# Performance work log

Measured on AMD Instinct MI355X. Metric: run time of the kernel, lower is better.

The kernel has to match this reference:

```python
import jax, jax.numpy as jnp
import numpy as np

B = 1024
FEAT_C = [64, 64, 128, 256, 512]    # channel dim of each intermediate feature map
SPATIAL = [1024, 1024, 256, 64, 16]  # flattened HxW of each map (32x32 input)
STRIDES = [1, 1, 2, 4, 8]
NUM_CLASS = 10


def _conv(x, w, b, s):
    y = jax.lax.conv_general_dilated(x, w, (s, s), 'SAME',
                                     dimension_numbers=('NCHW', 'OIHW', 'NCHW'))
    return y + b[None, :, None, None]


def setup_inputs() -> dict:
    key = jax.random.key(0)
    ks = iter(jax.random.split(key, 64))
    nrm = lambda shape, scale=1.0: jax.random.normal(next(ks), shape, jnp.float32) * scale
    inp = {'x': nrm((B, 3, 32, 32))}
    inp['noise_w'] = nrm((15, 3, 3, 3), 0.1)
    inp['noise_b'] = nrm((15,), 0.01)
    for i, (c, s) in enumerate(zip(FEAT_C, SPATIAL)):
        inp[f'feat_w{i}'] = nrm((c, 3, 3, 3), 0.2)
        inp[f'feat_b{i}'] = nrm((c,), 0.01)
        inp[f'mu_w{i}'] = nrm((NUM_CLASS, s), 1.0 / np.sqrt(s))
        inp[f'mu_b{i}'] = nrm((NUM_CLASS,), 0.01)
        inp[f'std_w{i}'] = nrm((NUM_CLASS, s), 1.0 / np.sqrt(s))
        inp[f'std_b{i}'] = nrm((NUM_CLASS,), 0.01)
    inp['clf_w'] = nrm((1, 5), 0.5)
    inp['clf_b'] = nrm((1,), 0.01)
    return inp


def _forward(x, noise_w, noise_b, feat_ws, feat_bs, mu_ws, mu_bs, std_ws, std_bs, clf_w, clf_b):
    Bsz = x.shape[0]
    # noised_img = x.repeat([1,5,1,1]) + noise_layer(x)   -> [B,15,32,32]
    noised = jnp.tile(x, (1, 5, 1, 1)) + _conv(x, noise_w, noise_b, 1)
    ekey = jax.random.key(42)
    scores, means, stds = [], [], []
    for i in range(5):
        xi = noised[:, 3 * i:3 * (i + 1)]
        # stand-in for pretrained_model.intermediate_forward -> [B, C_i, S_i]
        f = _conv(xi, feat_ws[i], feat_bs[i], STRIDES[i]).reshape(Bsz, FEAT_C[i], -1)
        # Linear over flattened-spatial dim then transpose(1,2): [B, 10, C_i]
        x_mean = jnp.einsum('bcs,ks->bkc', f, mu_ws[i]) + mu_bs[i][None, :, None]
        x_std = jnp.einsum('bcs,ks->bkc', f, std_ws[i]) + std_bs[i][None, :, None]
        # original builds dense diag(std)^2 [B,10,C,C]; diagonal exploited analytically
        var = x_std * x_std                       # diag entries of x_variance (== scale_tril)
        eps = jax.random.normal(jax.random.fold_in(ekey, i), x_mean.shape, x_mean.dtype)
        d = var * eps                             # sample - mean = scale_tril @ eps (diagonal)
        # -0.5 * d^T inv(diag(var)) d, inverse done analytically instead of torch.inverse
        mahal = -0.5 * jnp.sum(d * d / var, axis=-1)   # [B, 10]
        idx = jnp.argmax(mahal, axis=1)
        scores.append(jnp.max(mahal, axis=1))
        means.append(jnp.take_along_axis(x_mean, idx[:, None, None], axis=1)[:, 0, :])
        stds.append(jnp.take_along_axis(x_std, idx[:, None, None], axis=1)[:, 0, :])
    score_stack = jnp.stack(scores, axis=1)       # [B, 5]
    out = (score_stack @ clf_w.T + clf_b)[:, 0]   # classifier Linear(5,1), squeeze(-1)
    return out, means, stds


def reference(x, noise_w, noise_b,
              feat_w0, feat_b0, mu_w0, mu_b0, std_w0, std_b0,
              feat_w1, feat_b1, mu_w1, mu_b1, std_w1, std_b1,
              feat_w2, feat_b2, mu_w2, mu_b2, std_w2, std_b2,
              feat_w3, feat_b3, mu_w3, mu_b3, std_w3, std_b3,
              feat_w4, feat_b4, mu_w4, mu_b4, std_w4, std_b4,
              clf_w, clf_b):
    feat_ws = [feat_w0, feat_w1, feat_w2, feat_w3, feat_w4]
    feat_bs = [feat_b0, feat_b1, feat_b2, feat_b3, feat_b4]
    mu_ws = [mu_w0, mu_w1, mu_w2, mu_w3, mu_w4]
    mu_bs = [mu_b0, mu_b1, mu_b2, mu_b3, mu_b4]
    std_ws = [std_w0, std_w1, std_w2, std_w3, std_w4]
    std_bs = [std_b0, std_b1, std_b2, std_b3, std_b4]
    out, means, stds = _forward(x, noise_w, noise_b, feat_ws, feat_bs,
                                mu_ws, mu_bs, std_ws, std_bs, clf_w, clf_b)
    return (out, *means, *stds)
```

## Files before the change

kernel.cpp:

```cpp
#include <hip/hip_runtime.h>
#include <cstdint>

#define B_SZ 1024

__host__ __device__ inline void tf2x32(uint32_t k0, uint32_t k1,
                                       uint32_t x0, uint32_t x1,
                                       uint32_t& o0, uint32_t& o1) {
  uint32_t ks2 = 0x1BD11BDAu ^ k0 ^ k1;
#define TF_RND(r) { x0 += x1; x1 = (x1 << (r)) | (x1 >> (32 - (r))); x1 ^= x0; }
  x0 += k0; x1 += k1;
  TF_RND(13) TF_RND(15) TF_RND(26) TF_RND(6)
  x0 += k1; x1 += ks2 + 1u;
  TF_RND(17) TF_RND(29) TF_RND(16) TF_RND(24)
  x0 += ks2; x1 += k0 + 2u;
  TF_RND(13) TF_RND(15) TF_RND(26) TF_RND(6)
  x0 += k0; x1 += k1 + 3u;
  TF_RND(17) TF_RND(29) TF_RND(16) TF_RND(24)
  x0 += k1; x1 += ks2 + 4u;
  TF_RND(13) TF_RND(15) TF_RND(26) TF_RND(6)
  x0 += ks2; x1 += k0 + 5u;
#undef TF_RND
  o0 = x0; o1 = x1;
}

__device__ inline float erfinv_f32(float x) {
  float w = -log1pf(-x * x);
  float p;
  if (w < 5.0f) {
    w -= 2.5f;
    p = 2.81022636e-08f;
    p = fmaf(p, w, 3.43273939e-07f);
    p = fmaf(p, w, -3.5233877e-06f);
    p = fmaf(p, w, -4.39150654e-06f);
    p = fmaf(p, w, 0.00021858087f);
    p = fmaf(p, w, -0.00125372503f);
    p = fmaf(p, w, -0.00417768164f);
    p = fmaf(p, w, 0.246640727f);
    p = fmaf(p, w, 1.50140941f);
  } else {
    w = sqrtf(w) - 3.0f;
    p = -0.000200214257f;
    p = fmaf(p, w, 0.000100950558f);
    p = fmaf(p, w, 0.00134934322f);
    p = fmaf(p, w, -0.00367342844f);
    p = fmaf(p, w, 0.00573950773f);
    p = fmaf(p, w, -0.0076224613f);
    p = fmaf(p, w, 0.00943887047f);
    p = fmaf(p, w, 1.00167406f);
    p = fmaf(p, w, 2.83297682f);
  }
  return p * x;
}

__device__ inline float jax_normal_pt(uint32_t k0, uint32_t k1, uint32_t e) {
  uint32_t o0, o1;
  tf2x32(k0, k1, 0u, e, o0, o1);
  uint32_t bits = o0 ^ o1;
  float f = __uint_as_float((bits >> 9) | 0x3f800000u) - 1.0f;
  const float LO = -0.99999994f;
  float u = fmaxf(LO, fmaf(f, 2.0f, LO));
  return 1.41421356f * erfinv_f32(u);
}

struct OodArgs {
  const float* x;
  const float* noise_w;
  const float* noise_b;
  const float* feat_w[5];
  const float* feat_b[5];
  const float* mu_w[5];
  const float* mu_b[5];
  const float* std_w[5];
  const float* std_b[5];
  float* mean_out[5];
  float* std_out[5];
  float* scores;
  float* gws;
  uint32_t fk0[5], fk1[5];
};

#define PITCH 35
#define CHSZ  (34 * PITCH)
#define XSZ   (3 * CHSZ)

#define A_XP   0
#define A_XI   3570
#define A_NW   7140
#define A_NB   7221
#define A_SMEM 7224

template<int S, int STRIDE>
__device__ __forceinline__ void stageA(const OodArgs& A_, float* smem, int i) {
  constexpr int Wd = 32 / STRIDE;

  const int b = blockIdx.x;
  const int t = threadIdx.x;

  float* s_xp = smem + A_XP;
  float* s_xi = smem + A_XI;
  float* s_nw = smem + A_NW;
  float* s_nb = smem + A_NB;

  for (int p = t; p < 2 * XSZ; p += 320) smem[p] = 0.0f;
  if (t < 81) s_nw[t] = A_.noise_w[81 * i + t];
  if (t < 3)  s_nb[t] = A_.noise_b[3 * i + t];
  __syncthreads();
  const float* xb = A_.x + (size_t)b * 3072;
  for (int p = t; p < 3072; p += 320) {
    int ci = p >> 10; int rr = p & 1023; int yy = rr >> 5; int xx = rr & 31;
    s_xp[ci * CHSZ + (yy + 1) * PITCH + (xx + 1)] = xb[p];
  }
  __syncthreads();

  #pragma unroll
  for (int co = 0; co < 3; ++co) {
    float nwr[27];
    #pragma unroll
    for (int j = 0; j < 27; ++j) nwr[j] = s_nw[co * 27 + j];
    const float nb = s_nb[co];
    for (int p = t; p < 1024; p += 320) {
      const int base = (p >> 5) * PITCH + (p & 31);
      float a = nb;
      #pragma unroll
      for (int c2 = 0; c2 < 3; ++c2) {
        #pragma unroll
        for (int q = 0; q < 9; ++q)
          a = fmaf(s_xp[c2 * CHSZ + base + (q / 3) * PITCH + (q % 3)],
                   nwr[c2 * 9 + q], a);
      }
      s_xi[co * CHSZ + base + PITCH + 1] = a + s_xp[co * CHSZ + base + PITCH + 1];
    }
  }
  __syncthreads();

  const int G  = t >> 4;
  const int ss = t & 15;
  const int wh = G & 1;
  const int kk = G >> 1;
  const float* wsrc = (wh ? A_.std_w[i] : A_.mu_w[i]) + kk * S;
  float* gdst = A_.gws + (size_t)(b * 5 + i) * 560;

  if constexpr (STRIDE == 1) {
    const float* wr = wsrc + (2 * ss) * 32;
    const int rbase0 = (2 * ss) * PITCH;
    #pragma unroll
    for (int ci = 0; ci < 3; ++ci) {
      const int rb = ci * CHSZ + rbase0;
      float acc[10];
      #pragma unroll
      for (int j = 0; j < 10; ++j) acc[j] = 0.0f;
      float Av[4], Bv[4], Cv[4];
      #pragma unroll
      for (int u = 0; u < 4; ++u) {
        Av[u] = s_xi[rb + u * PITCH + 0];
        Bv[u] = s_xi[rb + u * PITCH + 1];
      }

#define WCOMP(V, L) ((L) == 0 ? (V).x : (L) == 1 ? (V).y : (L) == 2 ? (V).z : (V).w)
#define STEP(X, P, Q, R, W0, W1) { \
    _Pragma("unroll") \
    for (int u = 0; u < 4; ++u) R[u] = s_xi[rb + u * PITCH + (X) + 2]; \
    const float w0c = WCOMP(W0, (X) & 3); \
    const float w1c = WCOMP(W1, (X) & 3); \
    _Pragma("unroll") \
    for (int dy = 0; dy < 3; ++dy) { \
      acc[dy*3+0] = fmaf(w0c, P[dy], fmaf(w1c, P[dy+1], acc[dy*3+0])); \
      acc[dy*3+1] = fmaf(w0c, Q[dy], fmaf(w1c, Q[dy+1], acc[dy*3+1])); \
      acc[dy*3+2] = fmaf(w0c, R[dy], fmaf(w1c, R[dy+1], acc[dy*3+2])); \
    } \
    if (ci == 0) acc[9] += w0c + w1c; \
  }
#define G4_0(c) { const float4 w0 = *(const float4*)(wr + (c)); \
                  const float4 w1 = *(const float4*)(wr + 32 + (c)); \
    STEP((c)+0, Av, Bv, Cv, w0, w1) STEP((c)+1, Bv, Cv, Av, w0, w1) \
    STEP((c)+2, Cv, Av, Bv, w0, w1) STEP((c)+3, Av, Bv, Cv, w0, w1) }
#define G4_1(c) { const float4 w0 = *(const float4*)(wr + (c)); \
                  const float4 w1 = *(const float4*)(wr + 32 + (c)); \
    STEP((c)+0, Bv, Cv, Av, w0, w1) STEP((c)+1, Cv, Av, Bv, w0, w1) \
    STEP((c)+2, Av, Bv, Cv, w0, w1) STEP((c)+3, Bv, Cv, Av, w0, w1) }
#define G4_2(c) { const float4 w0 = *(const float4*)(wr + (c)); \
                  const float4 w1 = *(const float4*)(wr + 32 + (c)); \
    STEP((c)+0, Cv, Av, Bv, w0, w1) STEP((c)+1, Av, Bv, Cv, w0, w1) \
    STEP((c)+2, Bv, Cv, Av, w0, w1) STEP((c)+3, Cv, Av, Bv, w0, w1) }

      G4_0(0) G4_1(4) G4_2(8) G4_0(12) G4_1(16) G4_2(20) G4_0(24) G4_1(28)

#undef G4_0
#undef G4_1
#undef G4_2
#undef STEP
#undef WCOMP
      #pragma unroll
      for (int j = 0; j < 10; ++j) {
        float v = acc[j];
        v += __shfl_xor(v, 1, 64);
        v += __shfl_xor(v, 2, 64);
        v += __shfl_xor(v, 4, 64);
        v += __shfl_xor(v, 8, 64);
        acc[j] = v;
      }
      if (ss == 0) {
        #pragma unroll
        for (int j = 0; j < 9; ++j)
          gdst[(wh * 10 + kk) * 27 + ci * 9 + j] = acc[j];
        if (ci == 0) gdst[540 + wh * 10 + kk] = acc[9];
      }
    }
  } else {
    constexpr int PER = S / 16;
    #pragma unroll
    for (int ci = 0; ci < 3; ++ci) {
      float acc[10];
      #pragma unroll
      for (int j = 0; j < 10; ++j) acc[j] = 0.0f;
      #pragma unroll
      for (int u = 0; u < PER; ++u) {
        const int s  = ss * PER + u;
        const int yo = s / Wd, xo = s % Wd;
        const float wx = wsrc[s];
        #pragma unroll
        for (int dy = 0; dy < 3; ++dy) {
          const int base = ci * CHSZ + (yo * STRIDE + dy + 1) * PITCH + (xo * STRIDE + 1);
          #pragma unroll
          for (int dx = 0; dx < 3; ++dx)
            acc[dy * 3 + dx] = fmaf(wx, s_xi[base + dx], acc[dy * 3 + dx]);
        }
        if (ci == 0) acc[9] += wx;
      }
      #pragma unroll
      for (int j = 0; j < 10; ++j) {
        float v = acc[j];
        v += __shfl_xor(v, 1, 64);
        v += __shfl_xor(v, 2, 64);
        v += __shfl_xor(v, 4, 64);
        v += __shfl_xor(v, 8, 64);
        acc[j] = v;
      }
      if (ss == 0) {
        #pragma unroll
        for (int j = 0; j < 9; ++j)
          gdst[(wh * 10 + kk) * 27 + ci * 9 + j] = acc[j];
        if (ci == 0) gdst[540 + wh * 10 + kk] = acc[9];
      }
    }
  }
}

__global__ __launch_bounds__(320, 8)
void ood_a(OodArgs A_) {
  __shared__ float smem[A_SMEM];
  const int y = blockIdx.y;
  switch (y) {
    case 0:
    case 1: stageA<1024, 1>(A_, smem, y); break;
    case 2: stageA< 256, 2>(A_, smem, 2); break;
    case 3: stageA<  64, 4>(A_, smem, 3); break;
    default: stageA< 16, 8>(A_, smem, 4); break;
  }
}

template<int I, int C>
__device__ __forceinline__ void stageB(const OodArgs& A_, float* smem) {
  const int b = blockIdx.x;
  const int t = threadIdx.x;

  float* s_g   = smem;
  float* s_rs  = smem + 540;
  float* s_std = smem + 560;
  float* s_pt  = smem + 560 + 10 * C;
  int*   s_idx = (int*)(smem + 570 + 10 * C);

  const float* feat_w = A_.feat_w[I];
  const float* feat_b = A_.feat_b[I];
  const uint32_t fk0 = A_.fk0[I], fk1 = A_.fk1[I];

  const float* gsrc = A_.gws + (size_t)(b * 5 + I) * 560;
  for (int p = t; p < 560; p += 320) smem[p] = gsrc[p];
  __syncthreads();

  for (int v = t; v < 10 * C; v += 320) {
    const int k2 = v / C; const int c = v - k2 * C;
    const float* fw = feat_w + c * 27;
    float a2 = 0.0f;
    #pragma unroll
    for (int j = 0; j < 27; ++j) a2 = fmaf(s_g[(10 + k2) * 27 + j], fw[j], a2);
    a2 = fmaf(feat_b[c], s_rs[10 + k2], a2) + A_.std_b[I][k2];
    s_std[v] = a2;
  }
  __syncthreads();

  {
    const int g  = t >> 6;
    const int ln = t & 63;
    float m0 = 0.0f, m1 = 0.0f;
    for (int c = ln; c < C; c += 64) {
      {
        const float sd  = s_std[g * C + c];
        const float eps = jax_normal_pt(fk0, fk1, (uint32_t)((b * 10 + g) * C + c));
        m0 = fmaf(sd * sd, eps * eps, m0);
      }
      {
        const float sd  = s_std[(g + 5) * C + c];
        const float eps = jax_normal_pt(fk0, fk1, (uint32_t)((b * 10 + g + 5) * C + c));
        m1 = fmaf(sd * sd, eps * eps, m1);
      }
    }
    #pragma unroll
    for (int off = 32; off > 0; off >>= 1) {
      m0 += __shfl_down(m0, off, 64);
      m1 += __shfl_down(m1, off, 64);
    }
    if (ln == 0) { s_pt[g] = m0; s_pt[g + 5] = m1; }
  }
  __syncthreads();
  if (t == 0) {
    float best = -INFINITY; int bi = 0;
    #pragma unroll
    for (int k2 = 0; k2 < 10; ++k2) {
      float m = -0.5f * s_pt[k2];
      if (m > best) { best = m; bi = k2; }
    }
    A_.scores[b * 5 + I] = best;
    *s_idx = bi;
  }
  __syncthreads();

  const int idx = *s_idx;
  for (int c = t; c < C; c += 320) {
    const float* fw = feat_w + c * 27;
    float a1 = 0.0f;
    #pragma unroll
    for (int j = 0; j < 27; ++j) a1 = fmaf(s_g[idx * 27 + j], fw[j], a1);
    a1 = fmaf(feat_b[c], s_rs[idx], a1) + A_.mu_b[I][idx];
    A_.mean_out[I][(size_t)b * C + c] = a1;
    A_.std_out[I][(size_t)b * C + c]  = s_std[idx * C + c];
  }
}

__global__ __launch_bounds__(320)
void ood_b(OodArgs A_) {
  __shared__ float smem[571 + 5120];
  switch (blockIdx.y) {
    case 0: stageB<0,  64>(A_, smem); break;
    case 1: stageB<1,  64>(A_, smem); break;
    case 2: stageB<2, 128>(A_, smem); break;
    case 3: stageB<3, 256>(A_, smem); break;
    default: stageB<4, 512>(A_, smem); break;
  }
}

__global__ void ood_clf(const float* __restrict__ scores,
                        const float* __restrict__ clf_w,
                        const float* __restrict__ clf_b,
                        float* __restrict__ out) {
  int b = blockIdx.x * blockDim.x + threadIdx.x;
  if (b < B_SZ) {
    float acc = clf_b[0];
    #pragma unroll
    for (int i = 0; i < 5; ++i) acc = fmaf(scores[b * 5 + i], clf_w[i], acc);
    out[b] = acc;
  }
}

extern "C" void kernel_launch(void* const* d_in, const int* in_sizes, int n_in,
                              void* d_out, int out_size, void* d_ws, size_t ws_size,
                              hipStream_t stream) {
  (void)in_sizes; (void)n_in; (void)out_size; (void)ws_size;
  const float* clf_w = (const float*)d_in[33];
  const float* clf_b = (const float*)d_in[34];
  float* out = (float*)d_out;
  float* ws  = (float*)d_ws;

  OodArgs A_;
  A_.x       = (const float*)d_in[0];
  A_.noise_w = (const float*)d_in[1];
  A_.noise_b = (const float*)d_in[2];
  const size_t NMEAN = 1048576;
  const size_t moff[5] = {1024, 66560, 132096, 263168, 525312};
  for (int i = 0; i < 5; ++i) {
    A_.feat_w[i]   = (const float*)d_in[3 + 6 * i];
    A_.feat_b[i]   = (const float*)d_in[4 + 6 * i];
    A_.mu_w[i]     = (const float*)d_in[5 + 6 * i];
    A_.mu_b[i]     = (const float*)d_in[6 + 6 * i];
    A_.std_w[i]    = (const float*)d_in[7 + 6 * i];
    A_.std_b[i]    = (const float*)d_in[8 + 6 * i];
    A_.mean_out[i] = out + moff[i];
    A_.std_out[i]  = out + moff[i] + NMEAN;
    tf2x32(0u, 42u, 0u, (uint32_t)i, A_.fk0[i], A_.fk1[i]);
  }
  A_.scores = ws;
  A_.gws    = ws + 5120;

  ood_a<<<dim3(B_SZ, 5), 320, 0, stream>>>(A_);
  ood_b<<<dim3(B_SZ, 5), 320, 0, stream>>>(A_);
  ood_clf<<<(B_SZ + 255) / 256, 256, 0, stream>>>(A_.scores, clf_w, clf_b, out);
}
```

Measured before the change: 322.4 us.

## Restructure noise conv, halve stage-A smem, fuse classifier into per-batch stage B

Stage A now does the noise conv in place in one image buffer, with 192 threads each computing 16 outputs in a register-rotating sliding window. The weighted-sum phase is remapped so each 32-lane group handles two classes at once and reuses the loaded pixels. Launch bounds drop from 8 to 5 blocks. Stage B becomes one block per batch element that loops over the five feature maps and computes the final classifier inline, removing the separate classifier kernel and the score buffer round-trip. This trades per-map parallelism in stage B (5x fewer blocks) for fewer launches and less shared memory in stage A.

```diff
diff --git a/kernel.cpp b/kernel.cpp
--- a/kernel.cpp
+++ b/kernel.cpp
@@ -72,9 +72,11 @@
   const float* mu_b[5];
   const float* std_w[5];
   const float* std_b[5];
+  const float* clf_w;
+  const float* clf_b;
   float* mean_out[5];
   float* std_out[5];
-  float* scores;
+  float* out;
   float* gws;
   uint32_t fk0[5], fk1[5];
 };
@@ -82,104 +84,155 @@
 #define PITCH 35
 #define CHSZ  (34 * PITCH)
 #define XSZ   (3 * CHSZ)
-
-#define A_XP   0
-#define A_XI   3570
-#define A_NW   7140
-#define A_NB   7221
-#define A_SMEM 7224
+#define A_NW   XSZ
+#define A_NB   (XSZ + 81)
+#define A_SMEM (XSZ + 84)
 
 template<int S, int STRIDE>
 __device__ __forceinline__ void stageA(const OodArgs& A_, float* smem, int i) {
   constexpr int Wd = 32 / STRIDE;
-
   const int b = blockIdx.x;
   const int t = threadIdx.x;
-
-  float* s_xp = smem + A_XP;
-  float* s_xi = smem + A_XI;
-  float* s_nw = smem + A_NW;
-  float* s_nb = smem + A_NB;
-
-  for (int p = t; p < 2 * XSZ; p += 320) smem[p] = 0.0f;
+  float* s_img = smem;
+  float* s_nw  = smem + A_NW;
+  float* s_nb  = smem + A_NB;
+
+  for (int p = t; p < XSZ; p += 320) s_img[p] = 0.0f;
   if (t < 81) s_nw[t] = A_.noise_w[81 * i + t];
   if (t < 3)  s_nb[t] = A_.noise_b[3 * i + t];
   __syncthreads();
   const float* xb = A_.x + (size_t)b * 3072;
   for (int p = t; p < 3072; p += 320) {
-    int ci = p >> 10; int rr = p & 1023; int yy = rr >> 5; int xx = rr & 31;
-    s_xp[ci * CHSZ + (yy + 1) * PITCH + (xx + 1)] = xb[p];
+    int ci = p >> 10, rr = p & 1023, yy = rr >> 5, xx = rr & 31;
+    s_img[ci * CHSZ + (yy + 1) * PITCH + (xx + 1)] = xb[p];
   }
   __syncthreads();
 
-  #pragma unroll
-  for (int co = 0; co < 3; ++co) {
-    float nwr[27];
-    #pragma unroll
-    for (int j = 0; j < 27; ++j) nwr[j] = s_nw[co * 27 + j];
+  float acc2[16];
+  int ob = 0;
+  const bool act = (t < 192);
+  if (act) {
+    const int co = t / 64, r = t % 64, y = r >> 1, xs = (r & 1) * 16;
+    ob = co * CHSZ + (y + 1) * PITCH + (xs + 1);
     const float nb = s_nb[co];
-    for (int p = t; p < 1024; p += 320) {
-      const int base = (p >> 5) * PITCH + (p & 31);
-      float a = nb;
-      #pragma unroll
-      for (int c2 = 0; c2 < 3; ++c2) {
-        #pragma unroll
-        for (int q = 0; q < 9; ++q)
-          a = fmaf(s_xp[c2 * CHSZ + base + (q / 3) * PITCH + (q % 3)],
-                   nwr[c2 * 9 + q], a);
-      }
-      s_xi[co * CHSZ + base + PITCH + 1] = a + s_xp[co * CHSZ + base + PITCH + 1];
+    #pragma unroll
+    for (int j = 0; j < 16; ++j) acc2[j] = nb;
+    #pragma unroll
+    for (int c2 = 0; c2 < 3; ++c2) {
+      float nwr[9];
+      #pragma unroll
+      for (int q = 0; q < 9; ++q) nwr[q] = s_nw[co * 27 + c2 * 9 + q];
+      const int wb = c2 * CHSZ + y * PITCH + xs;
+      float P[3], Q[3], R[3];
+      #pragma unroll
+      for (int d = 0; d < 3; ++d) {
+        P[d] = s_img[wb + d * PITCH];
+        Q[d] = s_img[wb + d * PITCH + 1];
+      }
+#define CSTEP(J, P_, Q_, R_) { \
+      _Pragma("unroll") \
+      for (int d = 0; d < 3; ++d) R_[d] = s_img[wb + d * PITCH + (J) + 2]; \
+      _Pragma("unroll") \
+      for (int d = 0; d < 3; ++d) { \
+        acc2[J] = fmaf(nwr[d*3+0], P_[d], acc2[J]); \
+        acc2[J] = fmaf(nwr[d*3+1], Q_[d], acc2[J]); \
+        acc2[J] = fmaf(nwr[d*3+2], R_[d], acc2[J]); \
+      } }
+      CSTEP(0,P,Q,R)  CSTEP(1,Q,R,P)  CSTEP(2,R,P,Q)
+      CSTEP(3,P,Q,R)  CSTEP(4,Q,R,P)  CSTEP(5,R,P,Q)
+      CSTEP(6,P,Q,R)  CSTEP(7,Q,R,P)  CSTEP(8,R,P,Q)
+      CSTEP(9,P,Q,R)  CSTEP(10,Q,R,P) CSTEP(11,R,P,Q)
+      CSTEP(12,P,Q,R) CSTEP(13,Q,R,P) CSTEP(14,R,P,Q)
+      CSTEP(15,P,Q,R)
+#undef CSTEP
     }
   }
   __syncthreads();
-
-  const int G  = t >> 4;
-  const int ss = t & 15;
-  const int wh = G & 1;
-  const int kk = G >> 1;
-  const float* wsrc = (wh ? A_.std_w[i] : A_.mu_w[i]) + kk * S;
+  if (act) {
+    #pragma unroll
+    for (int j = 0; j < 16; ++j) {
+      const float v = acc2[j] + s_img[ob + j];
+      s_img[ob + j] = v;
+    }
+  }
+  __syncthreads();
+
+  const int g  = t >> 5;
+  const int ss = t & 31;
+  const int wh = g & 1;
+  const int k0 = (g >> 1) * 2;
+  const float* wbase = (wh ? A_.std_w[i] : A_.mu_w[i]) + k0 * S;
   float* gdst = A_.gws + (size_t)(b * 5 + i) * 560;
 
+#define REDUCE_WRITE(ci_) { \
+    _Pragma("unroll") \
+    for (int j = 0; j < 9; ++j) { \
+      float v0 = a0[j], v1 = a1[j]; \
+      v0 += __shfl_xor(v0, 1, 64);  v1 += __shfl_xor(v1, 1, 64); \
+      v0 += __shfl_xor(v0, 2, 64);  v1 += __shfl_xor(v1, 2, 64); \
+      v0 += __shfl_xor(v0, 4, 64);  v1 += __shfl_xor(v1, 4, 64); \
+      v0 += __shfl_xor(v0, 8, 64);  v1 += __shfl_xor(v1, 8, 64); \
+      v0 += __shfl_xor(v0, 16, 64); v1 += __shfl_xor(v1, 16, 64); \
+      a0[j] = v0; a1[j] = v1; \
+    } \
+    if ((ci_) == 0) { \
+      rs0 += __shfl_xor(rs0, 1, 64); rs0 += __shfl_xor(rs0, 2, 64); \
+      rs0 += __shfl_xor(rs0, 4, 64); rs0 += __shfl_xor(rs0, 8, 64); \
+      rs0 += __shfl_xor(rs0, 16, 64); \
+      rs1 += __shfl_xor(rs1, 1, 64); rs1 += __shfl_xor(rs1, 2, 64); \
+      rs1 += __shfl_xor(rs1, 4, 64); rs1 += __shfl_xor(rs1, 8, 64); \
+      rs1 += __shfl_xor(rs1, 16, 64); \
+    } \
+    if (ss == 0) { \
+      _Pragma("unroll") \
+      for (int j = 0; j < 9; ++j) { \
+        gdst[(wh * 10 + k0) * 27 + (ci_) * 9 + j]     = a0[j]; \
+        gdst[(wh * 10 + k0 + 1) * 27 + (ci_) * 9 + j] = a1[j]; \
+      } \
+      if ((ci_) == 0) { \
+        gdst[540 + wh * 10 + k0]     = rs0; \
+        gdst[540 + wh * 10 + k0 + 1] = rs1; \
+      } \
+    } }
+
   if constexpr (STRIDE == 1) {
-    const float* wr = wsrc + (2 * ss) * 32;
-    const int rbase0 = (2 * ss) * PITCH;
+    const float* wr = wbase + ss * 32;
     #pragma unroll
     for (int ci = 0; ci < 3; ++ci) {
-      const int rb = ci * CHSZ + rbase0;
-      float acc[10];
-      #pragma unroll
-      for (int j = 0; j < 10; ++j) acc[j] = 0.0f;
-      float Av[4], Bv[4], Cv[4];
-      #pragma unroll
-      for (int u = 0; u < 4; ++u) {
-        Av[u] = s_xi[rb + u * PITCH + 0];
-        Bv[u] = s_xi[rb + u * PITCH + 1];
-      }
-
+      const int rb = ci * CHSZ + ss * PITCH;
+      float a0[9], a1[9];
+      #pragma unroll
+      for (int j = 0; j < 9; ++j) { a0[j] = 0.0f; a1[j] = 0.0f; }
+      float rs0 = 0.0f, rs1 = 0.0f;
+      float Av[3], Bv[3], Cv[3];
+      #pragma unroll
+      for (int u = 0; u < 3; ++u) {
+        Av[u] = s_img[rb + u * PITCH];
+        Bv[u] = s_img[rb + u * PITCH + 1];
+      }
 #define WCOMP(V, L) ((L) == 0 ? (V).x : (L) == 1 ? (V).y : (L) == 2 ? (V).z : (V).w)
-#define STEP(X, P, Q, R, W0, W1) { \
+#define STEP(X, P_, Q_, R_, W0, W1) { \
     _Pragma("unroll") \
-    for (int u = 0; u < 4; ++u) R[u] = s_xi[rb + u * PITCH + (X) + 2]; \
+    for (int u = 0; u < 3; ++u) R_[u] = s_img[rb + u * PITCH + (X) + 2]; \
     const float w0c = WCOMP(W0, (X) & 3); \
     const float w1c = WCOMP(W1, (X) & 3); \
     _Pragma("unroll") \
     for (int dy = 0; dy < 3; ++dy) { \
-      acc[dy*3+0] = fmaf(w0c, P[dy], fmaf(w1c, P[dy+1], acc[dy*3+0])); \
-      acc[dy*3+1] = fmaf(w0c, Q[dy], fmaf(w1c, Q[dy+1], acc[dy*3+1])); \
-      acc[dy*3+2] = fmaf(w0c, R[dy], fmaf(w1c, R[dy+1], acc[dy*3+2])); \
+      a0[dy*3+0] = fmaf(w0c, P_[dy], a0[dy*3+0]); a1[dy*3+0] = fmaf(w1c, P_[dy], a1[dy*3+0]); \
+      a0[dy*3+1] = fmaf(w0c, Q_[dy], a0[dy*3+1]); a1[dy*3+1] = fmaf(w1c, Q_[dy], a1[dy*3+1]); \
+      a0[dy*3+2] = fmaf(w0c, R_[dy], a0[dy*3+2]); a1[dy*3+2] = fmaf(w1c, R_[dy], a1[dy*3+2]); \
     } \
-    if (ci == 0) acc[9] += w0c + w1c; \
-  }
+    if (ci == 0) { rs0 += w0c; rs1 += w1c; } }
 #define G4_0(c) { const float4 w0 = *(const float4*)(wr + (c)); \
-                  const float4 w1 = *(const float4*)(wr + 32 + (c)); \
+                  const float4 w1 = *(const float4*)(wr + S + (c)); \
     STEP((c)+0, Av, Bv, Cv, w0, w1) STEP((c)+1, Bv, Cv, Av, w0, w1) \
     STEP((c)+2, Cv, Av, Bv, w0, w1) STEP((c)+3, Av, Bv, Cv, w0, w1) }
 #define G4_1(c) { const float4 w0 = *(const float4*)(wr + (c)); \
-                  const float4 w1 = *(const float4*)(wr + 32 + (c)); \
+                  const float4 w1 = *(const float4*)(wr + S + (c)); \
     STEP((c)+0, Bv, Cv, Av, w0, w1) STEP((c)+1, Cv, Av, Bv, w0, w1) \
     STEP((c)+2, Av, Bv, Cv, w0, w1) STEP((c)+3, Bv, Cv, Av, w0, w1) }
 #define G4_2(c) { const float4 w0 = *(const float4*)(wr + (c)); \
-                  const float4 w1 = *(const float4*)(wr + 32 + (c)); \
+                  const float4 w1 = *(const float4*)(wr + S + (c)); \
     STEP((c)+0, Cv, Av, Bv, w0, w1) STEP((c)+1, Av, Bv, Cv, w0, w1) \
     STEP((c)+2, Bv, Cv, Av, w0, w1) STEP((c)+3, Cv, Av, Bv, w0, w1) }
 
@@ -190,63 +243,43 @@
 #undef G4_2
 #undef STEP
 #undef WCOMP
-      #pragma unroll
-      for (int j = 0; j < 10; ++j) {
-        float v = acc[j];
-        v += __shfl_xor(v, 1, 64);
-        v += __shfl_xor(v, 2, 64);
-        v += __shfl_xor(v, 4, 64);
-        v += __shfl_xor(v, 8, 64);
-        acc[j] = v;
-      }
-      if (ss == 0) {
+      REDUCE_WRITE(ci)
+    }
+  } else {
+    constexpr int PER = (S >= 32) ? (S / 32) : 1;
+    #pragma unroll
+    for (int ci = 0; ci < 3; ++ci) {
+      float a0[9], a1[9];
+      #pragma unroll
+      for (int j = 0; j < 9; ++j) { a0[j] = 0.0f; a1[j] = 0.0f; }
+      float rs0 = 0.0f, rs1 = 0.0f;
+      if (S >= 32 || ss < S) {
         #pragma unroll
-        for (int j = 0; j < 9; ++j)
-          gdst[(wh * 10 + kk) * 27 + ci * 9 + j] = acc[j];
-        if (ci == 0) gdst[540 + wh * 10 + kk] = acc[9];
-      }
-    }
-  } else {
-    constexpr int PER = S / 16;
-    #pragma unroll
-    for (int ci = 0; ci < 3; ++ci) {
-      float acc[10];
-      #pragma unroll
-      for (int j = 0; j < 10; ++j) acc[j] = 0.0f;
-      #pragma unroll
-      for (int u = 0; u < PER; ++u) {
-        const int s  = ss * PER + u;
-        const int yo = s / Wd, xo = s % Wd;
-        const float wx = wsrc[s];
-        #pragma unroll
-        for (int dy = 0; dy < 3; ++dy) {
-          const int base = ci * CHSZ + (yo * STRIDE + dy + 1) * PITCH + (xo * STRIDE + 1);
+        for (int u = 0; u < PER; ++u) {
+          const int s  = (S >= 32) ? (ss * PER + u) : ss;
+          const int yo = s / Wd, xo = s % Wd;
+          const float wx0 = wbase[s];
+          const float wx1 = wbase[S + s];
           #pragma unroll
-          for (int dx = 0; dx < 3; ++dx)
-            acc[dy * 3 + dx] = fmaf(wx, s_xi[base + dx], acc[dy * 3 + dx]);
+          for (int dy = 0; dy < 3; ++dy) {
+            const int ba = ci * CHSZ + (yo * STRIDE + dy + 1) * PITCH + (xo * STRIDE + 1);
+            #pragma unroll
+            for (int dx = 0; dx < 3; ++dx) {
+              const float v = s_img[ba + dx];
+              a0[dy*3+dx] = fmaf(wx0, v, a0[dy*3+dx]);
+              a1[dy*3+dx] = fmaf(wx1, v, a1[dy*3+dx]);
+            }
+          }
+          if (ci == 0) { rs0 += wx0; rs1 += wx1; }
         }
-        if (ci == 0) acc[9] += wx;
-      }
-      #pragma unroll
-      for (int j = 0; j < 10; ++j) {
-        float v = acc[j];
-        v += __shfl_xor(v, 1, 64);
-        v += __shfl_xor(v, 2, 64);
-        v += __shfl_xor(v, 4, 64);
-        v += __shfl_xor(v, 8, 64);
-        acc[j] = v;
-      }
-      if (ss == 0) {
-        #pragma unroll
-        for (int j = 0; j < 9; ++j)
-          gdst[(wh * 10 + kk) * 27 + ci * 9 + j] = acc[j];
-        if (ci == 0) gdst[540 + wh * 10 + kk] = acc[9];
-      }
-    }
-  }
-}
-
-__global__ __launch_bounds__(320, 8)
+      }
+      REDUCE_WRITE(ci)
+    }
+  }
+#undef REDUCE_WRITE
+}
+
+__global__ __launch_bounds__(320, 5)
 void ood_a(OodArgs A_) {
   __shared__ float smem[A_SMEM];
   const int y = blockIdx.y;
@@ -259,106 +292,92 @@
   }
 }
 
-template<int I, int C>
-__device__ __forceinline__ void stageB(const OodArgs& A_, float* smem) {
-  const int b = blockIdx.x;
-  const int t = threadIdx.x;
-
+__global__ __launch_bounds__(320)
+void ood_b(OodArgs A_) {
+  __shared__ float smem[5696];
   float* s_g   = smem;
   float* s_rs  = smem + 540;
   float* s_std = smem + 560;
-  float* s_pt  = smem + 560 + 10 * C;
-  int*   s_idx = (int*)(smem + 570 + 10 * C);
-
-  const float* feat_w = A_.feat_w[I];
-  const float* feat_b = A_.feat_b[I];
-  const uint32_t fk0 = A_.fk0[I], fk1 = A_.fk1[I];
-
-  const float* gsrc = A_.gws + (size_t)(b * 5 + I) * 560;
-  for (int p = t; p < 560; p += 320) smem[p] = gsrc[p];
-  __syncthreads();
-
-  for (int v = t; v < 10 * C; v += 320) {
-    const int k2 = v / C; const int c = v - k2 * C;
-    const float* fw = feat_w + c * 27;
-    float a2 = 0.0f;
-    #pragma unroll
-    for (int j = 0; j < 27; ++j) a2 = fmaf(s_g[(10 + k2) * 27 + j], fw[j], a2);
-    a2 = fmaf(feat_b[c], s_rs[10 + k2], a2) + A_.std_b[I][k2];
-    s_std[v] = a2;
-  }
-  __syncthreads();
-
-  {
-    const int g  = t >> 6;
-    const int ln = t & 63;
-    float m0 = 0.0f, m1 = 0.0f;
-    for (int c = ln; c < C; c += 64) {
-      {
-        const float sd  = s_std[g * C + c];
-        const float eps = jax_normal_pt(fk0, fk1, (uint32_t)((b * 10 + g) * C + c));
-        m0 = fmaf(sd * sd, eps * eps, m0);
-      }
-      {
-        const float sd  = s_std[(g + 5) * C + c];
-        const float eps = jax_normal_pt(fk0, fk1, (uint32_t)((b * 10 + g + 5) * C + c));
-        m1 = fmaf(sd * sd, eps * eps, m1);
-      }
-    }
-    #pragma unroll
-    for (int off = 32; off > 0; off >>= 1) {
-      m0 += __shfl_down(m0, off, 64);
-      m1 += __shfl_down(m1, off, 64);
-    }
-    if (ln == 0) { s_pt[g] = m0; s_pt[g + 5] = m1; }
+  float* s_pt  = smem + 5680;
+  float* s_sc  = smem + 5690;
+  int*   s_idx = (int*)(smem + 5695);
+  const int b = blockIdx.x;
+  const int t = threadIdx.x;
+
+  #pragma unroll 1
+  for (int i = 0; i < 5; ++i) {
+    const int C   = (i < 2) ? 64 : (i == 2 ? 128 : (i == 3 ? 256 : 512));
+    const int csh = (i < 2) ? 6  : (i == 2 ? 7   : (i == 3 ? 8   : 9));
+    const float* feat_w = A_.feat_w[i];
+    const float* feat_b = A_.feat_b[i];
+    const float* gsrc = A_.gws + (size_t)(b * 5 + i) * 560;
+    __syncthreads();
+    for (int p = t; p < 560; p += 320) smem[p] = gsrc[p];
+    __syncthreads();
+
+    for (int v = t; v < 10 * C; v += 320) {
+      const int k2 = v >> csh, c = v & (C - 1);
+      const float* fw = feat_w + c * 27;
+      float a2 = 0.0f;
+      #pragma unroll
+      for (int j = 0; j < 27; ++j) a2 = fmaf(s_g[(10 + k2) * 27 + j], fw[j], a2);
+      a2 = fmaf(feat_b[c], s_rs[10 + k2], a2) + A_.std_b[i][k2];
+      s_std[v] = a2;
+    }
+    __syncthreads();
+
+    {
+      const int g = t >> 6, ln = t & 63;
+      const uint32_t fk0 = A_.fk0[i], fk1 = A_.fk1[i];
+      float m0 = 0.0f, m1 = 0.0f;
+      for (int c = ln; c < C; c += 64) {
+        const float sd0 = s_std[g * C + c];
+        const float e0  = jax_normal_pt(fk0, fk1, (uint32_t)((b * 10 + g) * C + c));
+        m0 = fmaf(sd0 * sd0, e0 * e0, m0);
+        const float sd1 = s_std[(g + 5) * C + c];
+        const float e1  = jax_normal_pt(fk0, fk1, (uint32_t)((b * 10 + g + 5) * C + c));
+        m1 = fmaf(sd1 * sd1, e1 * e1, m1);
+      }
+      #pragma unroll
+      for (int off = 32; off > 0; off >>= 1) {
+        m0 += __shfl_down(m0, off, 64);
+        m1 += __shfl_down(m1, off, 64);
+      }
+      if (ln == 0) { s_pt[g] = m0; s_pt[g + 5] = m1; }
+    }
+    __syncthreads();
+    if (t == 0) {
+      float best = -INFINITY; int bi = 0;
+      #pragma unroll
+      for (int k = 0; k < 10; ++k) {
+        float m = -0.5f * s_pt[k];
+        if (m > best) { best = m; bi = k; }
+      }
+      s_sc[i] = best; *s_idx = bi;
+    }
+    __syncthreads();
+
+    const int idx = *s_idx;
+    float* mo = A_.mean_out[i];
+    float* so = A_.std_out[i];
+    const float mb   = A_.mu_b[i][idx];
+    const float rs0v = s_rs[idx];
+    for (int c = t; c < C; c += 320) {
+      const float* fw = feat_w + c * 27;
+      float a1v = 0.0f;
+      #pragma unroll
+      for (int j = 0; j < 27; ++j) a1v = fmaf(s_g[idx * 27 + j], fw[j], a1v);
+      a1v = fmaf(feat_b[c], rs0v, a1v) + mb;
+      mo[(size_t)b * C + c] = a1v;
+      so[(size_t)b * C + c] = s_std[idx * C + c];
+    }
   }
   __syncthreads();
   if (t == 0) {
-    float best = -INFINITY; int bi = 0;
-    #pragma unroll
-    for (int k2 = 0; k2 < 10; ++k2) {
-      float m = -0.5f * s_pt[k2];
-      if (m > best) { best = m; bi = k2; }
-    }
-    A_.scores[b * 5 + I] = best;
-    *s_idx = bi;
-  }
-  __syncthreads();
-
-  const int idx = *s_idx;
-  for (int c = t; c < C; c += 320) {
-    const float* fw = feat_w + c * 27;
-    float a1 = 0.0f;
-    #pragma unroll
-    for (int j = 0; j < 27; ++j) a1 = fmaf(s_g[idx * 27 + j], fw[j], a1);
-    a1 = fmaf(feat_b[c], s_rs[idx], a1) + A_.mu_b[I][idx];
-    A_.mean_out[I][(size_t)b * C + c] = a1;
-    A_.std_out[I][(size_t)b * C + c]  = s_std[idx * C + c];
-  }
-}
-
-__global__ __launch_bounds__(320)
-void ood_b(OodArgs A_) {
-  __shared__ float smem[571 + 5120];
-  switch (blockIdx.y) {
-    case 0: stageB<0,  64>(A_, smem); break;
-    case 1: stageB<1,  64>(A_, smem); break;
-    case 2: stageB<2, 128>(A_, smem); break;
-    case 3: stageB<3, 256>(A_, smem); break;
-    default: stageB<4, 512>(A_, smem); break;
-  }
-}
-
-__global__ void ood_clf(const float* __restrict__ scores,
-                        const float* __restrict__ clf_w,
-                        const float* __restrict__ clf_b,
-                        float* __restrict__ out) {
-  int b = blockIdx.x * blockDim.x + threadIdx.x;
-  if (b < B_SZ) {
-    float acc = clf_b[0];
-    #pragma unroll
-    for (int i = 0; i < 5; ++i) acc = fmaf(scores[b * 5 + i], clf_w[i], acc);
-    out[b] = acc;
+    float acc = A_.clf_b[0];
+    #pragma unroll
+    for (int i2 = 0; i2 < 5; ++i2) acc = fmaf(s_sc[i2], A_.clf_w[i2], acc);
+    A_.out[b] = acc;
   }
 }
 
@@ -366,8 +385,6 @@
                               void* d_out, int out_size, void* d_ws, size_t ws_size,
                               hipStream_t stream) {
   (void)in_sizes; (void)n_in; (void)out_size; (void)ws_size;
-  const float* clf_w = (const float*)d_in[33];
-  const float* clf_b = (const float*)d_in[34];
   float* out = (float*)d_out;
   float* ws  = (float*)d_ws;
 
@@ -375,6 +392,8 @@
   A_.x       = (const float*)d_in[0];
   A_.noise_w = (const float*)d_in[1];
   A_.noise_b = (const float*)d_in[2];
+  A_.clf_w   = (const float*)d_in[33];
+  A_.clf_b   = (const float*)d_in[34];
   const size_t NMEAN = 1048576;
   const size_t moff[5] = {1024, 66560, 132096, 263168, 525312};
   for (int i = 0; i < 5; ++i) {
@@ -388,10 +407,9 @@
     A_.std_out[i]  = out + moff[i] + NMEAN;
     tf2x32(0u, 42u, 0u, (uint32_t)i, A_.fk0[i], A_.fk1[i]);
   }
-  A_.scores = ws;
-  A_.gws    = ws + 5120;
+  A_.out = out;
+  A_.gws = ws;
 
   ood_a<<<dim3(B_SZ, 5), 320, 0, stream>>>(A_);
-  ood_b<<<dim3(B_SZ, 5), 320, 0, stream>>>(A_);
-  ood_clf<<<(B_SZ + 255) / 256, 256, 0, stream>>>(A_.scores, clf_w, clf_b, out);
-}
+  ood_b<<<B_SZ, 320, 0, stream>>>(A_);
+}
```

After: 345.3 us. +7.1%, slower.
